# Optimization experiments

Hardware: AMD Instinct MI355X
Metric: run time of the kernel (lower is better)

The kernel has to match this reference:

```python
import jax, jax.numpy as jnp
import numpy as np

# hyp2f1 parameters of the Mann eddy-lifetime model: 2F1(1/3, 17/6, 4/3, -(kL)^-2)
A_P = 1.0 / 3.0
B_P = 17.0 / 6.0
C_P = 4.0 / 3.0
N_TERMS = 1000  # series terms; tail ~ N^{-2.5} -> ~1e-8 rel. error


def _hyp2f1_pfaff_series(w):
    """2F1(1/3, -3/2, 4/3, w) for w in [0, 1] via its power series.

    This is the Pfaff-transformed series; terms decay like n^{-3.5} * w^n,
    so a fixed N_TERMS truncation is accurate over the whole range.
    """
    a, bp, c = A_P, C_P - B_P, C_P  # bp = -3/2

    def body(carry, n):
        s, term = carry
        term = term * ((a + n) * (bp + n)) / ((c + n) * (n + 1.0)) * w
        return (s + term, term), None

    init = (jnp.ones_like(w), jnp.ones_like(w))
    (s, _), _ = jax.lax.scan(body, init, jnp.arange(N_TERMS, dtype=w.dtype))
    return s


def _mann_hyp2f1(t):
    """2F1(1/3, 17/6, 4/3, -t^-2) for t > 0 via the Pfaff transformation.

    2F1(a,b,c,z) = (1-z)^{-a} 2F1(a, c-b, c, z/(z-1)) with z = -1/t^2,
    so z/(z-1) = 1/(1+t^2) in (0,1) and (1-z) = (1+t^2)/t^2.
    """
    t2 = t * t
    w = 1.0 / (1.0 + t2)
    pref = (t2 * w) ** A_P  # (1-z)^{-a}
    return pref * _hyp2f1_pfaff_series(w)


def setup_inputs() -> dict:
    key = jax.random.key(0)
    k = jax.random.normal(key, (256, 256, 128, 3), dtype=jnp.float32)
    L = jnp.ones((), dtype=jnp.float32)
    gamma = jnp.ones((), dtype=jnp.float32)
    return {"k": k, "L": L, "gamma": gamma}


def reference(k, L, gamma):
    # Original detaches k and L (tau is non-differentiable); only gamma carries grad.
    k_s = jax.lax.stop_gradient(k)
    L_s = jax.lax.stop_gradient(L)
    k_norm = jnp.linalg.norm(k_s, axis=-1)  # [256,256,128]
    kL = L_s * k_norm
    mask = kL > 0.0
    safe_t = jnp.where(mask, kL, 1.0)
    F = _mann_hyp2f1(safe_t)
    tau = jnp.where(mask, safe_t ** (-2.0 / 3.0) / jnp.sqrt(F), 0.0)
    return gamma * tau
```

## Files before the change

kernel.cpp:

```cpp
#include <hip/hip_runtime.h>
#include <math.h>


constexpr int NT = 64;

struct CoefArr { float v[NT]; };

constexpr CoefArr gen_coefs() {
    CoefArr r{};
    double term = 1.0;
    r.v[0] = 1.0f;
    for (int n = 0; n + 1 < NT; ++n) {
        const double a  = 1.0 / 3.0;
        const double bp = -1.5;
        const double c  = 4.0 / 3.0;
        term *= ((a + n) * (bp + n)) / ((c + n) * (n + 1.0));
        r.v[n + 1] = (float)term;
    }
    return r;
}

constexpr CoefArr COEF = gen_coefs();

__device__ __forceinline__ float mann_tau(float t2, float L_unused) {
    float w = 1.0f / (1.0f + t2);
    float s = COEF.v[NT - 1];
#pragma unroll
    for (int n = NT - 2; n >= 0; --n) s = fmaf(s, w, COEF.v[n]);
    float cw = exp2f(log2f(w) * (1.0f / 3.0f));
    return rsqrtf(t2 * cw * s);
}

__global__ __launch_bounds__(256) void mann_elt_kernel(
    const float* __restrict__ k,
    const float* __restrict__ Lp,
    const float* __restrict__ gp,
    float* __restrict__ out,
    int n)
{
    const int gid  = blockIdx.x * blockDim.x + threadIdx.x;
    const int base = gid * 4;
    if (base >= n) return;

    const float L  = Lp[0];
    const float g  = gp[0];
    const float L2 = L * L;

    if (base + 3 < n || (n & 3) == 0) {
        const float4* k4 = (const float4*)k + (size_t)gid * 3;
        float4 p0 = k4[0];
        float4 p1 = k4[1];
        float4 p2 = k4[2];

        float n2[4];
        n2[0] = fmaf(p0.x, p0.x, fmaf(p0.y, p0.y, p0.z * p0.z));
        n2[1] = fmaf(p0.w, p0.w, fmaf(p1.x, p1.x, p1.y * p1.y));
        n2[2] = fmaf(p1.z, p1.z, fmaf(p1.w, p1.w, p2.x * p2.x));
        n2[3] = fmaf(p2.y, p2.y, fmaf(p2.z, p2.z, p2.w * p2.w));

        float4 o;
        float* op = &o.x;
#pragma unroll
        for (int j = 0; j < 4; ++j) {
            float t2 = L2 * n2[j];
            float tau = mann_tau(t2, L);
            op[j] = (t2 > 0.0f) ? g * tau : 0.0f;
        }
        *(float4*)(out + base) = o;
    } else {
        for (int j = 0; j < 4 && base + j < n; ++j) {
            const int i = base + j;
            float kx = k[3 * (size_t)i + 0];
            float ky = k[3 * (size_t)i + 1];
            float kz = k[3 * (size_t)i + 2];
            float t2 = L2 * (kx * kx + ky * ky + kz * kz);
            float tau = mann_tau(t2, L);
            out[i] = (t2 > 0.0f) ? g * tau : 0.0f;
        }
    }
}

extern "C" void kernel_launch(void* const* d_in, const int* in_sizes, int n_in,
                              void* d_out, int out_size, void* d_ws, size_t ws_size,
                              hipStream_t stream) {
    const float* k  = (const float*)d_in[0];
    const float* L  = (const float*)d_in[1];
    const float* g  = (const float*)d_in[2];
    float* out = (float*)d_out;

    const int n  = out_size;
    const int n4 = (n + 3) / 4;
    const int block = 256;
    const int grid  = (n4 + block - 1) / block;

    mann_elt_kernel<<<grid, block, 0, stream>>>(k, L, g, out, n);
}
```

Baseline: 157.5 us.

## Cut series to 48 terms, use raw AMDGPU intrinsics, 8 elems/thread, nontemporal IO

```diff
diff --git a/kernel.cpp b/kernel.cpp
--- a/kernel.cpp
+++ b/kernel.cpp
@@ -2,7 +2,9 @@
 #include <math.h>
 
 
-constexpr int NT = 64;
+typedef float f4 __attribute__((ext_vector_type(4)));
+
+constexpr int NT = 48;
 
 struct CoefArr { float v[NT]; };
 
@@ -22,13 +24,13 @@
 
 constexpr CoefArr COEF = gen_coefs();
 
-__device__ __forceinline__ float mann_tau(float t2, float L_unused) {
-    float w = 1.0f / (1.0f + t2);
+__device__ __forceinline__ float mann_tau(float t2) {
+    float w = __builtin_amdgcn_rcpf(1.0f + t2);
     float s = COEF.v[NT - 1];
 #pragma unroll
     for (int n = NT - 2; n >= 0; --n) s = fmaf(s, w, COEF.v[n]);
-    float cw = exp2f(log2f(w) * (1.0f / 3.0f));
-    return rsqrtf(t2 * cw * s);
+    float cw = __builtin_amdgcn_exp2f(__builtin_amdgcn_logf(w) * (1.0f / 3.0f));
+    return __builtin_amdgcn_rsqf(t2 * cw * s);
 }
 
 __global__ __launch_bounds__(256) void mann_elt_kernel(
@@ -38,43 +40,50 @@
     float* __restrict__ out,
     int n)
 {
-    const int gid  = blockIdx.x * blockDim.x + threadIdx.x;
-    const int base = gid * 4;
+    const int  gid  = blockIdx.x * blockDim.x + threadIdx.x;
+    const long base = (long)gid * 8;
     if (base >= n) return;
 
     const float L  = Lp[0];
     const float g  = gp[0];
     const float L2 = L * L;
 
-    if (base + 3 < n || (n & 3) == 0) {
-        const float4* k4 = (const float4*)k + (size_t)gid * 3;
-        float4 p0 = k4[0];
-        float4 p1 = k4[1];
-        float4 p2 = k4[2];
+    if (base + 7 < (long)n) {
+        const f4* k4 = (const f4*)k + (size_t)gid * 6;
+        float f[24];
+#pragma unroll
+        for (int j = 0; j < 6; ++j) {
+            f4 v = __builtin_nontemporal_load(&k4[j]);
+            f[4 * j + 0] = v[0];
+            f[4 * j + 1] = v[1];
+            f[4 * j + 2] = v[2];
+            f[4 * j + 3] = v[3];
+        }
 
-        float n2[4];
-        n2[0] = fmaf(p0.x, p0.x, fmaf(p0.y, p0.y, p0.z * p0.z));
-        n2[1] = fmaf(p0.w, p0.w, fmaf(p1.x, p1.x, p1.y * p1.y));
-        n2[2] = fmaf(p1.z, p1.z, fmaf(p1.w, p1.w, p2.x * p2.x));
-        n2[3] = fmaf(p2.y, p2.y, fmaf(p2.z, p2.z, p2.w * p2.w));
+        float res[8];
+#pragma unroll
+        for (int j = 0; j < 8; ++j) {
+            float x = f[3 * j + 0];
+            float y = f[3 * j + 1];
+            float z = f[3 * j + 2];
+            float t2  = L2 * fmaf(x, x, fmaf(y, y, z * z));
+            float tau = mann_tau(t2);
+            res[j] = (t2 > 0.0f) ? g * tau : 0.0f;
+        }
 
-        float4 o;
-        float* op = &o.x;
-#pragma unroll
-        for (int j = 0; j < 4; ++j) {
-            float t2 = L2 * n2[j];
-            float tau = mann_tau(t2, L);
-            op[j] = (t2 > 0.0f) ? g * tau : 0.0f;
-        }
-        *(float4*)(out + base) = o;
+        f4 o0 = (f4){res[0], res[1], res[2], res[3]};
+        f4 o1 = (f4){res[4], res[5], res[6], res[7]};
+        f4* o4 = (f4*)(out + base);
+        __builtin_nontemporal_store(o0, o4 + 0);
+        __builtin_nontemporal_store(o1, o4 + 1);
     } else {
-        for (int j = 0; j < 4 && base + j < n; ++j) {
-            const int i = base + j;
-            float kx = k[3 * (size_t)i + 0];
-            float ky = k[3 * (size_t)i + 1];
-            float kz = k[3 * (size_t)i + 2];
-            float t2 = L2 * (kx * kx + ky * ky + kz * kz);
-            float tau = mann_tau(t2, L);
+        for (int j = 0; j < 8 && base + j < (long)n; ++j) {
+            const long i = base + j;
+            float kx = k[3 * i + 0];
+            float ky = k[3 * i + 1];
+            float kz = k[3 * i + 2];
+            float t2  = L2 * (kx * kx + ky * ky + kz * kz);
+            float tau = mann_tau(t2);
             out[i] = (t2 > 0.0f) ? g * tau : 0.0f;
         }
     }
@@ -89,9 +98,9 @@
     float* out = (float*)d_out;
 
     const int n  = out_size;
-    const int n4 = (n + 3) / 4;
+    const int n8 = (n + 7) / 8;
     const int block = 256;
-    const int grid  = (n4 + block - 1) / block;
+    const int grid  = (n8 + block - 1) / block;
 
     mann_elt_kernel<<<grid, block, 0, stream>>>(k, L, g, out, n);
 }
```

New measurement: 172.6 us. 1.1x slower.
